# Kernel optimization log

Measured on AMD Instinct MI355X. Metric: run time of the kernel, lower is better.

## Reference

```python
import jax, jax.numpy as jnp
import numpy as np
from jax import lax

CONTEXT = 7
EPS = 1e-5  # BatchNorm2d default eps
DN = ('NCHW', 'OIHW', 'NCHW')


def _cbr(x, W, b, g, be, m, v, padding):
    # conv2d + BatchNorm (eval, running stats) + ReLU
    y = lax.conv_general_dilated(x, W, (1, 1), padding, dimension_numbers=DN)
    y = y + b[None, :, None, None]
    y = (y - m[None, :, None, None]) * (g / jnp.sqrt(v + EPS))[None, :, None, None] + be[None, :, None, None]
    return jax.nn.relu(y)


def _pool21(x):  # MaxPool2d(kernel_size=(2,1))
    return lax.reduce_window(x, -jnp.inf, lax.max, (1, 1, 2, 1), (1, 1, 2, 1), 'VALID')


def setup_inputs() -> dict:
    key = jax.random.key(0)
    ks = jax.random.split(key, 16)
    B, T, F, NC = 16, 108, 144, 25
    d = {}
    d['x'] = jax.random.normal(ks[0], (B, T, F), jnp.float32)
    d['labels'] = jax.random.randint(ks[1], (B, T), 0, NC)
    shapes = [(32, 1, 3, 3), (32, 32, 3, 3), (32, 32, 3, 3), (32, 32, 3, 3),
              (64, 32, 3, 3), (64, 64, 3, 3), (128, 64, 12, 9)]
    for i, s in enumerate(shapes, 1):
        fan_in = s[1] * s[2] * s[3]
        d[f'W{i}'] = jax.random.normal(ks[1 + i], s, jnp.float32) / np.sqrt(fan_in).astype(np.float32)
        c = s[0]
        d[f'b{i}'] = jnp.zeros((c,), jnp.float32)
        d[f'g{i}'] = jnp.ones((c,), jnp.float32)
        d[f'be{i}'] = jnp.zeros((c,), jnp.float32)
        d[f'm{i}'] = jnp.zeros((c,), jnp.float32)
        d[f'v{i}'] = jnp.ones((c,), jnp.float32)
    d['W8'] = jax.random.normal(ks[9], (NC, 128, 1, 1), jnp.float32) / np.float32(np.sqrt(128.0))
    d['b8'] = jnp.zeros((NC,), jnp.float32)
    return d


def reference(x, labels,
              W1, b1, g1, be1, m1, v1,
              W2, b2, g2, be2, m2, v2,
              W3, b3, g3, be3, m3, v3,
              W4, b4, g4, be4, m4, v4,
              W5, b5, g5, be5, m5, v5,
              W6, b6, g6, be6, m6, v6,
              W7, b7, g7, be7, m7, v7,
              W8, b8):
    B, T, F = x.shape
    win_len = 2 * CONTEXT + 1
    # permute to [B, F, T], zero-pad time by CONTEXT on both sides
    xp = jnp.pad(jnp.transpose(x, (0, 2, 1)), ((0, 0), (0, 0), (CONTEXT, CONTEXT)))
    # vectorized sliding windows (replaces the nested python loop of slices+cat)
    idx = jnp.arange(T)[:, None] + jnp.arange(win_len)[None, :]  # [T, 15]
    win = xp[:, :, idx]                                          # [B, F, T, 15]
    h = jnp.transpose(win, (0, 2, 1, 3)).reshape(B * T, 1, F, win_len)
    h = _cbr(h, W1, b1, g1, be1, m1, v1, 'SAME')
    h = _cbr(h, W2, b2, g2, be2, m2, v2, 'SAME')
    h = _cbr(h, W3, b3, g3, be3, m3, v3, 'SAME')
    h = _cbr(h, W4, b4, g4, be4, m4, v4, 'SAME')
    h = _pool21(h)  # dropout2d is identity in eval
    h = _cbr(h, W5, b5, g5, be5, m5, v5, 'VALID')
    h = _cbr(h, W6, b6, g6, be6, m6, v6, 'VALID')
    h = _pool21(h)
    h = _cbr(h, W7, b7, g7, be7, m7, v7, 'VALID')
    h = lax.conv_general_dilated(h, W8, (1, 1), 'VALID', dimension_numbers=DN) + b8[None, :, None, None]
    logits = jnp.mean(h, axis=(2, 3))  # AvgPool2d over full spatial extent
    return logits.reshape(B, T, -1)    # probs_out=True -> CRF input
```

## Files before the change

kernel.cpp:

```cpp
#include <hip/hip_runtime.h>
#include <hip/hip_bf16.h>
#include <hip/hip_fp16.h>

#define TA 71680
#define SLOT 108544
#define C6N 23936

typedef _Float16 v8h __attribute__((ext_vector_type(8)));
typedef float v4f __attribute__((ext_vector_type(4)));
typedef unsigned short u16x8 __attribute__((ext_vector_type(8)));

__device__ inline float h2f(unsigned short u) {
    union { unsigned short s; _Float16 h; } v; v.s = u; return (float)v.h;
}
__device__ inline unsigned short f2h(float f) {
    union { unsigned short s; _Float16 h; } v; v.h = (_Float16)f; return v.s;
}

__global__ void repack_k(const float* __restrict__ W, const float* __restrict__ bb,
                         const float* __restrict__ gg, const float* __restrict__ be,
                         const float* __restrict__ mm, const float* __restrict__ vv,
                         float* __restrict__ wOut, float* __restrict__ tOut,
                         int CIN, int KHW, int COUT)
{
    int gid = blockIdx.x * 256 + threadIdx.x;
    if (gid < COUT) {
        float s = gg[gid] * rsqrtf(vv[gid] + 1e-5f);
        tOut[gid] = (bb[gid] - mm[gid]) * s + be[gid];
    }
    int tot = CIN * KHW * COUT;
    if (gid >= tot) return;
    int co = gid % COUT;
    int rest = gid / COUT;
    int k = rest % KHW;
    int ci = rest / KHW;
    float s = gg[co] * rsqrtf(vv[co] + 1e-5f);
    wOut[gid] = W[(co * CIN + ci) * KHW + k] * s;
}

__global__ void repack_mfma_k(const float* __restrict__ W, const float* __restrict__ bb,
                              const float* __restrict__ gg, const float* __restrict__ be,
                              const float* __restrict__ mm, const float* __restrict__ vv,
                              unsigned short* __restrict__ frag, float* __restrict__ tOut,
                              int CIN, int NT, int HALVES)
{
    int gid = blockIdx.x * 256 + threadIdx.x;
    int COUT = NT * 16;
    if (gid < COUT) {
        float s = gg[gid] * rsqrtf(vv[gid] + 1e-5f);
        tOut[gid] = (bb[gid] - mm[gid]) * s + be[gid];
    }
    int tot = 9 * HALVES * NT * 512;
    if (gid >= tot) return;
    int j    = gid & 7;
    int lane = (gid >> 3) & 63;
    int nt   = (gid >> 9) % NT;
    int rest = (gid >> 9) / NT;
    int half = rest % HALVES;
    int khw  = rest / HALVES;
    int ci   = half * 32 + (lane >> 4) * 8 + j;
    int co   = nt * 16 + (lane & 15);
    int kh   = khw / 3, kw = khw % 3;
    float s = gg[co] * rsqrtf(vv[co] + 1e-5f);
    frag[gid] = f2h(W[((co * CIN + ci) * 3 + kh) * 3 + kw] * s);
}

__global__ void repack7_k(const float* __restrict__ W, const float* __restrict__ bb,
                          const float* __restrict__ gg, const float* __restrict__ be,
                          const float* __restrict__ mm, const float* __restrict__ vv,
                          unsigned short* __restrict__ frag, float* __restrict__ tOut)
{
    int gid = blockIdx.x * 256 + threadIdx.x;
    if (gid < 128) {
        float s = gg[gid] * rsqrtf(vv[gid] + 1e-5f);
        tOut[gid] = (bb[gid] - mm[gid]) * s + be[gid];
    }
    if (gid >= 884736) return;
    int j    = gid & 7;
    int lane = (gid >> 3) & 63;
    int nt   = (gid >> 9) & 7;
    int half = (gid >> 12) & 1;
    int khw  = gid >> 13;
    int co   = nt * 16 + (lane & 15);
    int ci   = half * 32 + (lane >> 4) * 8 + j;
    int kh   = khw / 9, kw = khw - kh * 9;
    float s = gg[co] * rsqrtf(vv[co] + 1e-5f);
    frag[gid] = f2h(W[((co * 64 + ci) * 12 + kh) * 9 + kw] * s);
}

__global__ __launch_bounds__(256) void conv1_k(
    const float* __restrict__ x, unsigned short* __restrict__ out,
    const float* __restrict__ wr, const float* __restrict__ tv,
    int c0, int cn)
{
    int gid = blockIdx.x * 256 + threadIdx.x;
    if (gid >= cn * 2160) return;
    int nl = gid / 2160, p = gid - nl * 2160;
    int f = p / 15, w = p - f * 15;
    int n = c0 + nl;
    int b = n / 108, t = n - b * 108;

    float acc[32];
#pragma unroll
    for (int i = 0; i < 32; ++i) acc[i] = 0.f;

    for (int kh = 0; kh < 3; ++kh) {
        int ff = f + kh - 1;
        if (ff < 0 || ff >= 144) continue;
        for (int kw = 0; kw < 3; ++kw) {
            int c = w + kw - 1;
            if (c < 0 || c >= 15) continue;
            int tt = t + c - 7;
            if (tt < 0 || tt >= 108) continue;
            float xval = x[(b * 108 + tt) * 144 + ff];
            const float* wp = wr + (kh * 3 + kw) * 32;
#pragma unroll
            for (int q = 0; q < 8; ++q) {
                float4 wv = *(const float4*)(wp + q * 4);
                acc[q * 4 + 0] = fmaf(xval, wv.x, acc[q * 4 + 0]);
                acc[q * 4 + 1] = fmaf(xval, wv.y, acc[q * 4 + 1]);
                acc[q * 4 + 2] = fmaf(xval, wv.z, acc[q * 4 + 2]);
                acc[q * 4 + 3] = fmaf(xval, wv.w, acc[q * 4 + 3]);
            }
        }
    }
    unsigned short* ob = out + (size_t)nl * SLOT + (f * 15 + w) * 8;
#pragma unroll
    for (int cg = 0; cg < 4; ++cg) {
        u16x8 pk;
#pragma unroll
        for (int c = 0; c < 8; ++c)
            pk[c] = f2h(fmaxf(acc[cg * 8 + c] + tv[cg * 8 + c], 0.f));
        *(u16x8*)(ob + cg * 17280) = pk;
    }
}

__global__ __launch_bounds__(256) void conv234f_k(
    const unsigned short* __restrict__ in, unsigned short* __restrict__ out,
    const unsigned short* __restrict__ f2, const unsigned short* __restrict__ f3,
    const unsigned short* __restrict__ f4, const float* __restrict__ t2,
    const float* __restrict__ t3, const float* __restrict__ t4)
{
    __shared__ __align__(16) unsigned short sm[22912];
    const int band = blockIdx.x;
    const int n = blockIdx.y;
    const int tid = threadIdx.x;
    const int wave = tid >> 6, lane = tid & 63;
    const int m = lane & 15, quad = lane >> 4;

    {
        const float4* src = (const float4*)(in + (size_t)n * SLOT);
        float4* dst = (float4*)sm;
        const float4 z = {0.f, 0.f, 0.f, 0.f};
        for (int i = tid; i < 1656; i += 256) {
            if (i < 1496) {
                int q = i / 374, pos = i - q * 374;
                int r = pos / 17, c = pos - r * 17;
                int gr = band * 16 + r - 3;
                int gc = c - 1;
                float4 v = z;
                if (gr >= 0 && gr < 144 && gc >= 0 && gc < 15)
                    v = src[q * 2160 + gr * 15 + gc];
                dst[q * 375 + pos + (r > 0 ? r : 0) * 0 + r * 0 + 0 + (pos - pos)] = v;
                dst[q * 375 + pos] = v;
            } else {
                int j = i - 1496;
                int q = j / 40, jj = j - q * 40;
                int rr = jj >> 1, c2 = (jj & 1) * 16;
                dst[1500 + q * 341 + rr * 17 + c2] = z;
            }
        }
    }
    __syncthreads();

    v4f acc[2][5];
    int mt[5], la[5];

#pragma unroll
    for (int wt = 0; wt < 5; ++wt) {
        int t = wave * 5 + wt; if (t > 18) t = 18;
        mt[wt] = t;
        int p = t * 16 + m; if (p >= 300) p = 299;
        int r = p / 15, c = p - r * 15;
        la[wt] = r * 17 + c;
    }
#pragma unroll
    for (int nt = 0; nt < 2; ++nt)
#pragma unroll
        for (int wt = 0; wt < 5; ++wt) acc[nt][wt] = (v4f){0.f,0.f,0.f,0.f};
#pragma unroll
    for (int khw = 0; khw < 9; ++khw) {
        const int sh = (khw / 3) * 17 + (khw % 3);
        v8h a[5];
#pragma unroll
        for (int wt = 0; wt < 5; ++wt)
            a[wt] = *(const v8h*)(sm + quad * 3000 + (la[wt] + sh) * 8);
#pragma unroll
        for (int nt = 0; nt < 2; ++nt) {
            v8h b = *(const v8h*)(f2 + (khw * 2 + nt) * 512 + lane * 8);
#pragma unroll
            for (int wt = 0; wt < 5; ++wt)
                acc[nt][wt] = __builtin_amdgcn_mfma_f32_16x16x32_f16(a[wt], b, acc[nt][wt], 0, 0, 0);
        }
    }
#pragma unroll
    for (int wt = 0; wt < 5; ++wt) {
        const int pb = mt[wt] * 16 + quad * 4;
#pragma unroll
        for (int nt = 0; nt < 2; ++nt) {
            const int co = nt * 16 + m;
            const float tb = t2[co];
            unsigned short* ob = sm + 12000 + (co >> 3) * 2728 + (co & 7);
#pragma unroll
            for (int reg = 0; reg < 4; ++reg) {
                int p = pb + reg;
                if (p < 300) {
                    int r = p / 15, c = p - r * 15;
                    ob[(r * 17 + c + 1) * 8] = f2h(fmaxf(acc[nt][wt][reg] + tb, 0.f));
                }
            }
        }
    }
    __syncthreads();

    if (tid < 144) {
        int q = tid / 36, jj = tid - q * 36;
        int rr = jj >> 1, c2 = (jj & 1) * 16;
        *(float4*)((float4*)sm + q * 307 + rr * 17 + c2) = (float4){0.f,0.f,0.f,0.f};
    }

#pragma unroll
    for (int wt = 0; wt < 5; ++wt) {
        int t = wave * 5 + wt; if (t > 16) t = 16;
        mt[wt] = t;
        int p = t * 16 + m; if (p >= 270) p = 269;
        int r = p / 15, c = p - r * 15;
        la[wt] = r * 17 + c;
    }
#pragma unroll
    for (int nt = 0; nt < 2; ++nt)
#pragma unroll
        for (int wt = 0; wt < 5; ++wt) acc[nt][wt] = (v4f){0.f,0.f,0.f,0.f};
#pragma unroll
    for (int khw = 0; khw < 9; ++khw) {
        const int sh = (khw / 3) * 17 + (khw % 3);
        v8h a[5];
#pragma unroll
        for (int wt = 0; wt < 5; ++wt)
            a[wt] = *(const v8h*)(sm + 12000 + quad * 2728 + (la[wt] + sh) * 8);
#pragma unroll
        for (int nt = 0; nt < 2; ++nt) {
            v8h b = *(const v8h*)(f3 + (khw * 2 + nt) * 512 + lane * 8);
#pragma unroll
            for (int wt = 0; wt < 5; ++wt)
                acc[nt][wt] = __builtin_amdgcn_mfma_f32_16x16x32_f16(a[wt], b, acc[nt][wt], 0, 0, 0);
        }
    }
#pragma unroll
    for (int wt = 0; wt < 5; ++wt) {
        const int pb = mt[wt] * 16 + quad * 4;
#pragma unroll
        for (int nt = 0; nt < 2; ++nt) {
            const int co = nt * 16 + m;
            const float tb = t3[co];
            unsigned short* ob = sm + (co >> 3) * 2456 + (co & 7);
#pragma unroll
            for (int reg = 0; reg < 4; ++reg) {
                int p = pb + reg;
                if (p < 270) {
                    int r = p / 15, c = p - r * 15;
                    ob[(r * 17 + c + 1) * 8] = f2h(fmaxf(acc[nt][wt][reg] + tb, 0.f));
                }
            }
        }
    }
    __syncthreads();

    int mt4[4], la4[4];
#pragma unroll
    for (int wt = 0; wt < 4; ++wt) {
        int t = wave * 4 + wt; if (t > 14) t = 14;
        mt4[wt] = t;
        int p = t * 16 + m;
        int pr = p / 30, rem = p - pr * 30;
        int w = rem >> 1, r4 = pr * 2 + (rem & 1);
        la4[wt] = r4 * 17 + w;
    }
    v4f acc4[2][4];
#pragma unroll
    for (int nt = 0; nt < 2; ++nt)
#pragma unroll
        for (int wt = 0; wt < 4; ++wt) acc4[nt][wt] = (v4f){0.f,0.f,0.f,0.f};
#pragma unroll
    for (int khw = 0; khw < 9; ++khw) {
        const int sh = (khw / 3) * 17 + (khw % 3);
        v8h a[4];
#pragma unroll
        for (int wt = 0; wt < 4; ++wt)
            a[wt] = *(const v8h*)(sm + quad * 2456 + (la4[wt] + sh) * 8);
#pragma unroll
        for (int nt = 0; nt < 2; ++nt) {
            v8h b = *(const v8h*)(f4 + (khw * 2 + nt) * 512 + lane * 8);
#pragma unroll
            for (int wt = 0; wt < 4; ++wt)
                acc4[nt][wt] = __builtin_amdgcn_mfma_f32_16x16x32_f16(a[wt], b, acc4[nt][wt], 0, 0, 0);
        }
    }
    unsigned short* outN = out + (size_t)n * SLOT;
#pragma unroll
    for (int wt = 0; wt < 4; ++wt) {
        const int pb = band * 240 + mt4[wt] * 16 + quad * 4;
#pragma unroll
        for (int nt = 0; nt < 2; ++nt) {
            const int co = nt * 16 + m;
            const float tb = t4[co];
            unsigned short* ob = outN + (co >> 3) * 9216 + (co & 7);
#pragma unroll
            for (int pi = 0; pi < 2; ++pi) {
                int pe = pb + pi * 2;
                int pr = pe / 30, rem = pe - pr * 30, w = rem >> 1;
                float v0 = fmaxf(acc4[nt][wt][pi * 2] + tb, 0.f);
                float v1 = fmaxf(acc4[nt][wt][pi * 2 + 1] + tb, 0.f);
                ob[(pr * 16 + w) * 8] = f2h(fmaxf(v0, v1));
            }
        }
    }
}

__global__ __launch_bounds__(256) void conv5m_k(
    const unsigned short* __restrict__ in, unsigned short* __restrict__ out,
    const unsigned short* __restrict__ frag, const float* __restrict__ tv)
{
    const int n = blockIdx.y;
    const int tid = threadIdx.x;
    const int wave = tid >> 6, lane = tid & 63;
    const int m = lane & 15, quad = lane >> 4;
    const unsigned short* inN = in + (size_t)n * SLOT + quad * 9216;

    int mt[2], a0[2];
#pragma unroll
    for (int wt = 0; wt < 2; ++wt) {
        int t = blockIdx.x * 8 + wave * 2 + wt; if (t > 56) t = 56;
        mt[wt] = t;
        int p = t * 16 + m; if (p > 909) p = 909;
        int r = p / 13, w = p - r * 13;
        a0[wt] = (r * 16 + w) * 8;
    }

    v4f acc[4][2];
#pragma unroll
    for (int nt = 0; nt < 4; ++nt)
#pragma unroll
        for (int wt = 0; wt < 2; ++wt) acc[nt][wt] = (v4f){0.f,0.f,0.f,0.f};

#pragma unroll
    for (int khw = 0; khw < 9; ++khw) {
        const int shift = ((khw / 3) * 16 + (khw % 3)) * 8;
        v8h a[2];
#pragma unroll
        for (int wt = 0; wt < 2; ++wt)
            a[wt] = *(const v8h*)(inN + a0[wt] + shift);
#pragma unroll
        for (int nt = 0; nt < 4; ++nt) {
            v8h b = *(const v8h*)(frag + (khw * 4 + nt) * 512 + lane * 8);
#pragma unroll
            for (int wt = 0; wt < 2; ++wt)
                acc[nt][wt] = __builtin_amdgcn_mfma_f32_16x16x32_f16(a[wt], b, acc[nt][wt], 0, 0, 0);
        }
    }

    unsigned short* outN = out + (size_t)n * SLOT;
#pragma unroll
    for (int wt = 0; wt < 2; ++wt) {
        const int pb = mt[wt] * 16 + quad * 4;
#pragma unroll
        for (int nt = 0; nt < 4; ++nt) {
            const int co = nt * 16 + m;
            const float tb = tv[co];
            unsigned short* ob = outN + (co >> 3) * 8960 + (co & 7);
#pragma unroll
            for (int reg = 0; reg < 4; ++reg) {
                int p = pb + reg;
                if (p < 910) {
                    int r = p / 13, w = p - r * 13;
                    ob[(r * 16 + w) * 8] = f2h(fmaxf(acc[nt][wt][reg] + tb, 0.f));
                }
            }
        }
    }
}

__global__ __launch_bounds__(256) void conv6m_k(
    const unsigned short* __restrict__ in, unsigned short* __restrict__ c6,
    const unsigned short* __restrict__ frag, const float* __restrict__ tv)
{
    const int n = blockIdx.y;
    const int tid = threadIdx.x;
    const int wave = tid >> 6, lane = tid & 63;
    const int m = lane & 15, quad = lane >> 4;
    const unsigned short* inN = in + (size_t)n * SLOT;

    int mt[2], a0[2];
#pragma unroll
    for (int wt = 0; wt < 2; ++wt) {
        int t = blockIdx.x * 8 + wave * 2 + wt; if (t > 46) t = 46;
        mt[wt] = t;
        int p = t * 16 + m; if (p > 747) p = 747;
        int pr = p / 22, rem = p - pr * 22;
        int w = rem >> 1, r = pr * 2 + (rem & 1);
        a0[wt] = (r * 16 + w) * 8;
    }

    v4f acc[4][2];
#pragma unroll
    for (int nt = 0; nt < 4; ++nt)
#pragma unroll
        for (int wt = 0; wt < 2; ++wt) acc[nt][wt] = (v4f){0.f,0.f,0.f,0.f};

#pragma unroll
    for (int khw = 0; khw < 9; ++khw) {
        const int shift = ((khw / 3) * 16 + (khw % 3)) * 8;
#pragma unroll
        for (int half = 0; half < 2; ++half) {
            const unsigned short* ip = inN + (half * 4 + quad) * 8960 + shift;
            v8h a[2];
#pragma unroll
            for (int wt = 0; wt < 2; ++wt)
                a[wt] = *(const v8h*)(ip + a0[wt]);
#pragma unroll
            for (int nt = 0; nt < 4; ++nt) {
                v8h b = *(const v8h*)(frag + ((khw * 2 + half) * 4 + nt) * 512 + lane * 8);
#pragma unroll
                for (int wt = 0; wt < 2; ++wt)
                    acc[nt][wt] = __builtin_amdgcn_mfma_f32_16x16x32_f16(a[wt], b, acc[nt][wt], 0, 0, 0);
            }
        }
    }

    unsigned short* outN = c6 + (size_t)n * C6N;
#pragma unroll
    for (int wt = 0; wt < 2; ++wt) {
        const int pb = mt[wt] * 16 + quad * 4;
#pragma unroll
        for (int nt = 0; nt < 4; ++nt) {
            const int co = nt * 16 + m;
            const float tb = tv[co];
            unsigned short* ob = outN + (co >> 3) * 2992 + (co & 7);
#pragma unroll
            for (int pi = 0; pi < 2; ++pi) {
                int pe = pb + pi * 2;
                if (pe < 748) {
                    int pr = pe / 22, rem = pe - pr * 22, w = rem >> 1;
                    float v0 = fmaxf(acc[nt][wt][pi * 2] + tb, 0.f);
                    float v1 = fmaxf(acc[nt][wt][pi * 2 + 1] + tb, 0.f);
                    ob[(pr * 11 + w) * 8] = f2h(fmaxf(v0, v1));
                }
            }
        }
    }
}

__global__ __launch_bounds__(256) void conv7mfma_k(
    const unsigned short* __restrict__ c6, float* __restrict__ pooled,
    const unsigned short* __restrict__ frag7, const float* __restrict__ tv)
{
    __shared__ __align__(16) unsigned short sA[11968];
    const int n = blockIdx.x;
    const int tid = threadIdx.x;
    const int wave = tid >> 6;
    const int lane = tid & 63;
    const int m = lane & 15;
    const int quad = lane >> 4;

    int pm[5];
#pragma unroll
    for (int mt = 0; mt < 5; ++mt) {
        int p = mt * 16 + m;
        if (p >= 69) p = 0;
        pm[mt] = (p / 3) * 11 + (p % 3);
    }

    v4f acc[2][5];
#pragma unroll
    for (int t = 0; t < 2; ++t)
#pragma unroll
        for (int mt = 0; mt < 5; ++mt)
            acc[t][mt] = (v4f){0.f, 0.f, 0.f, 0.f};

    for (int half = 0; half < 2; ++half) {
        __syncthreads();
        {
            const float4* src = (const float4*)(c6 + (size_t)n * C6N + half * 11968);
            float4* dst = (float4*)sA;
            for (int i = tid; i < 1496; i += 256) dst[i] = src[i];
        }
        __syncthreads();
        for (int khw = 0; khw < 108; ++khw) {
            const int off = (khw / 9) * 11 + (khw % 9);
            v8h a[5];
#pragma unroll
            for (int mt = 0; mt < 5; ++mt)
                a[mt] = *(const v8h*)(sA + quad * 2992 + (pm[mt] + off) * 8);
            const unsigned short* bp = frag7
                + ((size_t)(khw * 2 + half) * 8) * 512 + lane * 8;
#pragma unroll
            for (int t = 0; t < 2; ++t) {
                const int nt = wave + t * 4;
                v8h b = *(const v8h*)(bp + nt * 512);
#pragma unroll
                for (int mt = 0; mt < 5; ++mt)
                    acc[t][mt] = __builtin_amdgcn_mfma_f32_16x16x32_f16(
                        a[mt], b, acc[t][mt], 0, 0, 0);
            }
        }
    }

    float s[2] = {0.f, 0.f};
#pragma unroll
    for (int t = 0; t < 2; ++t) {
        const float tb = tv[(wave + t * 4) * 16 + m];
#pragma unroll
        for (int mt = 0; mt < 5; ++mt) {
#pragma unroll
            for (int rr = 0; rr < 4; ++rr) {
                int p = mt * 16 + quad * 4 + rr;
                if (p < 69) s[t] += fmaxf(acc[t][mt][rr] + tb, 0.f);
            }
        }
    }
#pragma unroll
    for (int t = 0; t < 2; ++t) {
        s[t] += __shfl_xor(s[t], 16);
        s[t] += __shfl_xor(s[t], 32);
    }
    if (lane < 16) {
#pragma unroll
        for (int t = 0; t < 2; ++t)
            pooled[(size_t)n * 128 + (wave + t * 4) * 16 + lane] = s[t] * (1.f / 69.f);
    }
}

__global__ void logits_k(const float* __restrict__ pooled, const float* __restrict__ W8,
                         const float* __restrict__ b8, float* __restrict__ outg,
                         int total)
{
    int gid = blockIdx.x * 256 + threadIdx.x;
    if (gid >= total * 25) return;
    int nl = gid / 25, c = gid - nl * 25;
    const float* pp = pooled + (size_t)nl * 128;
    const float* wp = W8 + c * 128;
    float s = b8[c];
#pragma unroll
    for (int ci = 0; ci < 128; ci += 4) {
        float4 wv = *(const float4*)(wp + ci);
        float4 pv = *(const float4*)(pp + ci);
        s = fmaf(wv.x, pv.x, s);
        s = fmaf(wv.y, pv.y, s);
        s = fmaf(wv.z, pv.z, s);
        s = fmaf(wv.w, pv.w, s);
    }
    outg[(size_t)nl * 25 + c] = s;
}

extern "C" void kernel_launch(void* const* d_in, const int* in_sizes, int n_in,
                              void* d_out, int out_size, void* d_ws, size_t ws_size,
                              hipStream_t stream)
{
    const float* x = (const float*)d_in[0];
    const float* Wl[8]; const float* bl[8]; const float* gl[8];
    const float* bel[8]; const float* ml[8]; const float* vl[8];
    for (int i = 1; i <= 7; ++i) {
        int o = 2 + (i - 1) * 6;
        Wl[i]  = (const float*)d_in[o + 0];
        bl[i]  = (const float*)d_in[o + 1];
        gl[i]  = (const float*)d_in[o + 2];
        bel[i] = (const float*)d_in[o + 3];
        ml[i]  = (const float*)d_in[o + 4];
        vl[i]  = (const float*)d_in[o + 5];
    }
    const float* W8 = (const float*)d_in[44];
    const float* b8 = (const float*)d_in[45];
    float* ws = (float*)d_ws;

    float* wr1 = ws + 0;        float* t1 = ws + 288;
    unsigned short* f2b = (unsigned short*)(ws + 320);
    float* t2 = ws + 4928;
    unsigned short* f3b = (unsigned short*)(ws + 4960);
    float* t3 = ws + 9568;
    unsigned short* f4b = (unsigned short*)(ws + 9600);
    float* t4 = ws + 14208;
    unsigned short* f5b = (unsigned short*)(ws + 14240);
    float* t5 = ws + 23456;
    unsigned short* f6b = (unsigned short*)(ws + 23520);
    float* t6 = ws + 41952;
    unsigned short* f7b = (unsigned short*)(ws + 42016);
    float* t7 = ws + 484384;
    const size_t WFL = 484512;

    unsigned short* c6buf = (unsigned short*)(ws + WFL);
    const size_t C6FL = (size_t)1728 * C6N / 2;
    float* pooled = ws + WFL + C6FL;
    const size_t FIXED = WFL + C6FL + (size_t)1728 * 128;

    size_t avail_fl = ws_size / 4;
    size_t buf_halves = (avail_fl > FIXED) ? (avail_fl - FIXED) * 2 : 0;
    int Cs = (int)(buf_halves / (size_t)SLOT);
    if (Cs < 1) Cs = 1;
    if (Cs > 1728) Cs = 1728;
    unsigned short* bufA = (unsigned short*)(ws + FIXED);
    unsigned short* bufB = bufA + TA;

    auto g1 = [](int t) { return (t + 255) / 256; };

    repack_k<<<g1(288), 256, 0, stream>>>(Wl[1], bl[1], gl[1], bel[1], ml[1], vl[1], wr1, t1, 1, 9, 32);
    repack_mfma_k<<<g1(9216),  256, 0, stream>>>(Wl[2], bl[2], gl[2], bel[2], ml[2], vl[2], f2b, t2, 32, 2, 1);
    repack_mfma_k<<<g1(9216),  256, 0, stream>>>(Wl[3], bl[3], gl[3], bel[3], ml[3], vl[3], f3b, t3, 32, 2, 1);
    repack_mfma_k<<<g1(9216),  256, 0, stream>>>(Wl[4], bl[4], gl[4], bel[4], ml[4], vl[4], f4b, t4, 32, 2, 1);
    repack_mfma_k<<<g1(18432), 256, 0, stream>>>(Wl[5], bl[5], gl[5], bel[5], ml[5], vl[5], f5b, t5, 32, 4, 1);
    repack_mfma_k<<<g1(36864), 256, 0, stream>>>(Wl[6], bl[6], gl[6], bel[6], ml[6], vl[6], f6b, t6, 64, 4, 2);
    repack7_k<<<g1(884736), 256, 0, stream>>>(Wl[7], bl[7], gl[7], bel[7], ml[7], vl[7], f7b, t7);

    for (int c0 = 0; c0 < 1728; c0 += Cs) {
        int cn = (1728 - c0 < Cs) ? (1728 - c0) : Cs;
        conv1_k<<<g1(cn * 2160), 256, 0, stream>>>(x, bufA, wr1, t1, c0, cn);
        conv234f_k<<<dim3(9, cn), 256, 0, stream>>>(bufA, bufB, f2b, f3b, f4b, t2, t3, t4);
        conv5m_k<<<dim3(8, cn), 256, 0, stream>>>(bufB, bufA, f5b, t5);
        conv6m_k<<<dim3(6, cn), 256, 0, stream>>>(bufA, c6buf + (size_t)c0 * C6N, f6b, t6);
    }

    conv7mfma_k<<<1728, 256, 0, stream>>>(c6buf, pooled, f7b, t7);
    logits_k<<<g1(1728 * 25), 256, 0, stream>>>(pooled, W8, b8, (float*)d_out, 1728);
}
```

Baseline: 1.134 ms.

## Fuse conv1 into conv2-4 kernel and pad conv7 LDS rows

```diff
diff --git a/kernel.cpp b/kernel.cpp
--- a/kernel.cpp
+++ b/kernel.cpp
@@ -88,87 +88,81 @@
     frag[gid] = f2h(W[((co * 64 + ci) * 12 + kh) * 9 + kw] * s);
 }
 
-__global__ __launch_bounds__(256) void conv1_k(
+__global__ __launch_bounds__(256) void conv1234f_k(
     const float* __restrict__ x, unsigned short* __restrict__ out,
-    const float* __restrict__ wr, const float* __restrict__ tv,
-    int c0, int cn)
-{
-    int gid = blockIdx.x * 256 + threadIdx.x;
-    if (gid >= cn * 2160) return;
-    int nl = gid / 2160, p = gid - nl * 2160;
-    int f = p / 15, w = p - f * 15;
-    int n = c0 + nl;
-    int b = n / 108, t = n - b * 108;
-
-    float acc[32];
-#pragma unroll
-    for (int i = 0; i < 32; ++i) acc[i] = 0.f;
-
-    for (int kh = 0; kh < 3; ++kh) {
-        int ff = f + kh - 1;
-        if (ff < 0 || ff >= 144) continue;
-        for (int kw = 0; kw < 3; ++kw) {
-            int c = w + kw - 1;
-            if (c < 0 || c >= 15) continue;
-            int tt = t + c - 7;
-            if (tt < 0 || tt >= 108) continue;
-            float xval = x[(b * 108 + tt) * 144 + ff];
-            const float* wp = wr + (kh * 3 + kw) * 32;
-#pragma unroll
-            for (int q = 0; q < 8; ++q) {
-                float4 wv = *(const float4*)(wp + q * 4);
-                acc[q * 4 + 0] = fmaf(xval, wv.x, acc[q * 4 + 0]);
-                acc[q * 4 + 1] = fmaf(xval, wv.y, acc[q * 4 + 1]);
-                acc[q * 4 + 2] = fmaf(xval, wv.z, acc[q * 4 + 2]);
-                acc[q * 4 + 3] = fmaf(xval, wv.w, acc[q * 4 + 3]);
-            }
-        }
-    }
-    unsigned short* ob = out + (size_t)nl * SLOT + (f * 15 + w) * 8;
-#pragma unroll
-    for (int cg = 0; cg < 4; ++cg) {
-        u16x8 pk;
-#pragma unroll
-        for (int c = 0; c < 8; ++c)
-            pk[c] = f2h(fmaxf(acc[cg * 8 + c] + tv[cg * 8 + c], 0.f));
-        *(u16x8*)(ob + cg * 17280) = pk;
-    }
-}
-
-__global__ __launch_bounds__(256) void conv234f_k(
-    const unsigned short* __restrict__ in, unsigned short* __restrict__ out,
+    const float* __restrict__ wr1, const float* __restrict__ t1v,
     const unsigned short* __restrict__ f2, const unsigned short* __restrict__ f3,
     const unsigned short* __restrict__ f4, const float* __restrict__ t2,
-    const float* __restrict__ t3, const float* __restrict__ t4)
-{
-    __shared__ __align__(16) unsigned short sm[22912];
+    const float* __restrict__ t3, const float* __restrict__ t4, int c0)
+{
+    __shared__ __align__(16) unsigned short sm[23728];
+    float* sx = (float*)(sm + 22912);
     const int band = blockIdx.x;
-    const int n = blockIdx.y;
+    const int nl = blockIdx.y;
+    const int n = c0 + nl;
     const int tid = threadIdx.x;
     const int wave = tid >> 6, lane = tid & 63;
     const int m = lane & 15, quad = lane >> 4;
+    const int b = n / 108, t = n - b * 108;
 
     {
-        const float4* src = (const float4*)(in + (size_t)n * SLOT);
         float4* dst = (float4*)sm;
-        const float4 z = {0.f, 0.f, 0.f, 0.f};
-        for (int i = tid; i < 1656; i += 256) {
-            if (i < 1496) {
-                int q = i / 374, pos = i - q * 374;
-                int r = pos / 17, c = pos - r * 17;
-                int gr = band * 16 + r - 3;
-                int gc = c - 1;
-                float4 v = z;
-                if (gr >= 0 && gr < 144 && gc >= 0 && gc < 15)
-                    v = src[q * 2160 + gr * 15 + gc];
-                dst[q * 375 + pos + (r > 0 ? r : 0) * 0 + r * 0 + 0 + (pos - pos)] = v;
-                dst[q * 375 + pos] = v;
+        for (int i = tid; i < 568; i += 256) {
+            if (i < 408) {
+                int tp = i / 24, fp = i - tp * 24;
+                int tt = t - 8 + tp;
+                int ff = band * 16 - 4 + fp;
+                float v = 0.f;
+                if (tt >= 0 && tt < 108 && ff >= 0 && ff < 144)
+                    v = x[(b * 108 + tt) * 144 + ff];
+                sx[tp * 24 + fp] = v;
             } else {
-                int j = i - 1496;
+                int j = i - 408;
                 int q = j / 40, jj = j - q * 40;
                 int rr = jj >> 1, c2 = (jj & 1) * 16;
-                dst[1500 + q * 341 + rr * 17 + c2] = z;
-            }
+                dst[1500 + q * 341 + rr * 17 + c2] = (float4){0.f,0.f,0.f,0.f};
+            }
+        }
+    }
+    __syncthreads();
+
+    for (int e = tid; e < 374; e += 256) {
+        int r = e / 17, cp = e - r * 17;
+        int gr = band * 16 - 3 + r;
+        int gc = cp - 1;
+        float acc1[32];
+#pragma unroll
+        for (int i = 0; i < 32; ++i) acc1[i] = 0.f;
+        bool valid = (gr >= 0 && gr < 144 && gc >= 0 && gc < 15);
+        if (valid) {
+#pragma unroll
+            for (int kh = 0; kh < 3; ++kh) {
+                int fp = r + kh;
+#pragma unroll
+                for (int kw = 0; kw < 3; ++kw) {
+                    int c = gc + kw - 1;
+                    if (c < 0 || c >= 15) continue;
+                    float xv = sx[(c + 1) * 24 + fp];
+                    const float* wp = wr1 + (kh * 3 + kw) * 32;
+#pragma unroll
+                    for (int q8 = 0; q8 < 8; ++q8) {
+                        float4 wv = *(const float4*)(wp + q8 * 4);
+                        acc1[q8 * 4 + 0] = fmaf(xv, wv.x, acc1[q8 * 4 + 0]);
+                        acc1[q8 * 4 + 1] = fmaf(xv, wv.y, acc1[q8 * 4 + 1]);
+                        acc1[q8 * 4 + 2] = fmaf(xv, wv.z, acc1[q8 * 4 + 2]);
+                        acc1[q8 * 4 + 3] = fmaf(xv, wv.w, acc1[q8 * 4 + 3]);
+                    }
+                }
+            }
+        }
+#pragma unroll
+        for (int q2 = 0; q2 < 4; ++q2) {
+            u16x8 pk;
+#pragma unroll
+            for (int c8 = 0; c8 < 8; ++c8)
+                pk[c8] = valid ? f2h(fmaxf(acc1[q2 * 8 + c8] + t1v[q2 * 8 + c8], 0.f))
+                               : (unsigned short)0;
+            *(u16x8*)(sm + q2 * 3000 + (r * 17 + cp) * 8) = pk;
         }
     }
     __syncthreads();
@@ -178,9 +172,9 @@
 
 #pragma unroll
     for (int wt = 0; wt < 5; ++wt) {
-        int t = wave * 5 + wt; if (t > 18) t = 18;
-        mt[wt] = t;
-        int p = t * 16 + m; if (p >= 300) p = 299;
+        int tt = wave * 5 + wt; if (tt > 18) tt = 18;
+        mt[wt] = tt;
+        int p = tt * 16 + m; if (p >= 300) p = 299;
         int r = p / 15, c = p - r * 15;
         la[wt] = r * 17 + c;
     }
@@ -197,10 +191,10 @@
             a[wt] = *(const v8h*)(sm + quad * 3000 + (la[wt] + sh) * 8);
 #pragma unroll
         for (int nt = 0; nt < 2; ++nt) {
-            v8h b = *(const v8h*)(f2 + (khw * 2 + nt) * 512 + lane * 8);
+            v8h bb = *(const v8h*)(f2 + (khw * 2 + nt) * 512 + lane * 8);
 #pragma unroll
             for (int wt = 0; wt < 5; ++wt)
-                acc[nt][wt] = __builtin_amdgcn_mfma_f32_16x16x32_f16(a[wt], b, acc[nt][wt], 0, 0, 0);
+                acc[nt][wt] = __builtin_amdgcn_mfma_f32_16x16x32_f16(a[wt], bb, acc[nt][wt], 0, 0, 0);
         }
     }
 #pragma unroll
@@ -231,9 +225,9 @@
 
 #pragma unroll
     for (int wt = 0; wt < 5; ++wt) {
-        int t = wave * 5 + wt; if (t > 16) t = 16;
-        mt[wt] = t;
-        int p = t * 16 + m; if (p >= 270) p = 269;
+        int tt = wave * 5 + wt; if (tt > 16) tt = 16;
+        mt[wt] = tt;
+        int p = tt * 16 + m; if (p >= 270) p = 269;
         int r = p / 15, c = p - r * 15;
         la[wt] = r * 17 + c;
     }
@@ -250,10 +244,10 @@
             a[wt] = *(const v8h*)(sm + 12000 + quad * 2728 + (la[wt] + sh) * 8);
 #pragma unroll
         for (int nt = 0; nt < 2; ++nt) {
-            v8h b = *(const v8h*)(f3 + (khw * 2 + nt) * 512 + lane * 8);
+            v8h bb = *(const v8h*)(f3 + (khw * 2 + nt) * 512 + lane * 8);
 #pragma unroll
             for (int wt = 0; wt < 5; ++wt)
-                acc[nt][wt] = __builtin_amdgcn_mfma_f32_16x16x32_f16(a[wt], b, acc[nt][wt], 0, 0, 0);
+                acc[nt][wt] = __builtin_amdgcn_mfma_f32_16x16x32_f16(a[wt], bb, acc[nt][wt], 0, 0, 0);
         }
     }
 #pragma unroll
@@ -279,9 +273,9 @@
     int mt4[4], la4[4];
 #pragma unroll
     for (int wt = 0; wt < 4; ++wt) {
-        int t = wave * 4 + wt; if (t > 14) t = 14;
-        mt4[wt] = t;
-        int p = t * 16 + m;
+        int tt = wave * 4 + wt; if (tt > 14) tt = 14;
+        mt4[wt] = tt;
+        int p = tt * 16 + m;
         int pr = p / 30, rem = p - pr * 30;
         int w = rem >> 1, r4 = pr * 2 + (rem & 1);
         la4[wt] = r4 * 17 + w;
@@ -300,13 +294,13 @@
             a[wt] = *(const v8h*)(sm + quad * 2456 + (la4[wt] + sh) * 8);
 #pragma unroll
         for (int nt = 0; nt < 2; ++nt) {
-            v8h b = *(const v8h*)(f4 + (khw * 2 + nt) * 512 + lane * 8);
+            v8h bb = *(const v8h*)(f4 + (khw * 2 + nt) * 512 + lane * 8);
 #pragma unroll
             for (int wt = 0; wt < 4; ++wt)
-                acc4[nt][wt] = __builtin_amdgcn_mfma_f32_16x16x32_f16(a[wt], b, acc4[nt][wt], 0, 0, 0);
-        }
-    }
-    unsigned short* outN = out + (size_t)n * SLOT;
+                acc4[nt][wt] = __builtin_amdgcn_mfma_f32_16x16x32_f16(a[wt], bb, acc4[nt][wt], 0, 0, 0);
+        }
+    }
+    unsigned short* outN = out + (size_t)nl * SLOT;
 #pragma unroll
     for (int wt = 0; wt < 4; ++wt) {
         const int pb = band * 240 + mt4[wt] * 16 + quad * 4;
@@ -464,7 +458,7 @@
     const unsigned short* __restrict__ c6, float* __restrict__ pooled,
     const unsigned short* __restrict__ frag7, const float* __restrict__ tv)
 {
-    __shared__ __align__(16) unsigned short sA[11968];
+    __shared__ __align__(16) unsigned short sA[14176];
     const int n = blockIdx.x;
     const int tid = threadIdx.x;
     const int wave = tid >> 6;
@@ -477,7 +471,7 @@
     for (int mt = 0; mt < 5; ++mt) {
         int p = mt * 16 + m;
         if (p >= 69) p = 0;
-        pm[mt] = (p / 3) * 11 + (p % 3);
+        pm[mt] = (p / 3) * 13 + (p % 3);
     }
 
     v4f acc[2][5];
@@ -492,15 +486,19 @@
         {
             const float4* src = (const float4*)(c6 + (size_t)n * C6N + half * 11968);
             float4* dst = (float4*)sA;
-            for (int i = tid; i < 1496; i += 256) dst[i] = src[i];
+            for (int i = tid; i < 1496; i += 256) {
+                int q = i / 374, pos = i - q * 374;
+                int h = pos / 11, w = pos - h * 11;
+                dst[q * 443 + h * 13 + w] = src[i];
+            }
         }
         __syncthreads();
         for (int khw = 0; khw < 108; ++khw) {
-            const int off = (khw / 9) * 11 + (khw % 9);
+            const int off = (khw / 9) * 13 + (khw % 9);
             v8h a[5];
 #pragma unroll
             for (int mt = 0; mt < 5; ++mt)
-                a[mt] = *(const v8h*)(sA + quad * 2992 + (pm[mt] + off) * 8);
+                a[mt] = *(const v8h*)(sA + (quad * 443 + pm[mt] + off) * 8);
             const unsigned short* bp = frag7
                 + ((size_t)(khw * 2 + half) * 8) * 512 + lane * 8;
 #pragma unroll
@@ -622,8 +620,8 @@
 
     for (int c0 = 0; c0 < 1728; c0 += Cs) {
         int cn = (1728 - c0 < Cs) ? (1728 - c0) : Cs;
-        conv1_k<<<g1(cn * 2160), 256, 0, stream>>>(x, bufA, wr1, t1, c0, cn);
-        conv234f_k<<<dim3(9, cn), 256, 0, stream>>>(bufA, bufB, f2b, f3b, f4b, t2, t3, t4);
+        conv1234f_k<<<dim3(9, cn), 256, 0, stream>>>(x, bufB, wr1, t1,
+                                                     f2b, f3b, f4b, t2, t3, t4, c0);
         conv5m_k<<<dim3(8, cn), 256, 0, stream>>>(bufB, bufA, f5b, t5);
         conv6m_k<<<dim3(6, cn), 256, 0, stream>>>(bufA, c6buf + (size_t)c0 * C6N, f6b, t6);
     }
```

Result: no change. 1.130 ms (-0.3%).
